# Kernel tuning notes

Hardware: AMD Instinct MI355X
Metric: run time of the kernel (lower is better)

The kernel has to match this reference:

```python
import jax, jax.numpy as jnp
import numpy as np

Q_DIM = 1024
K_DIM = 1024
HID = 128
EPS = 1e-5


def setup_inputs() -> dict:
    key = jax.random.key(0)
    ks = jax.random.split(key, 12)
    B, Tq, Tk = 2, 512, 512
    s_q = 1.0 / np.sqrt(Q_DIM)
    s_k = 1.0 / np.sqrt(K_DIM)
    s_h3 = 1.0 / np.sqrt(3 * HID)
    s_h = 1.0 / np.sqrt(HID)
    return {
        "Q": jax.random.normal(ks[0], (B, Tq, Q_DIM), jnp.float32),
        "K": jax.random.normal(ks[1], (B, Tk, K_DIM), jnp.float32),
        "Wq": jax.random.uniform(ks[2], (Q_DIM, HID), jnp.float32, -s_q, s_q),
        "Wk": jax.random.uniform(ks[3], (K_DIM, HID), jnp.float32, -s_k, s_k),
        "ln_g": jnp.ones((3 * HID,), jnp.float32),
        "ln_b": jnp.zeros((3 * HID,), jnp.float32),
        "Wu": jax.random.uniform(ks[4], (3 * HID, HID), jnp.float32, -s_h3, s_h3),
        "bu": jax.random.uniform(ks[5], (HID,), jnp.float32, -s_h3, s_h3),
        "Wv": jax.random.uniform(ks[6], (3 * HID, HID), jnp.float32, -s_h3, s_h3),
        "bv": jax.random.uniform(ks[7], (HID,), jnp.float32, -s_h3, s_h3),
        "Wo": jax.random.uniform(ks[8], (HID, 1), jnp.float32, -s_h, s_h),
        "bo": jax.random.uniform(ks[9], (1,), jnp.float32, -s_h, s_h),
    }


def reference(Q, K, Wq, Wk, ln_g, ln_b, Wu, bu, Wv, bv, Wo, bo):
    B, Tq, _ = Q.shape
    Tk = K.shape[1]
    q = jnp.einsum("bqd,dh->bqh", Q, Wq)              # (B,Tq,H)
    k = jnp.einsum("bkd,dh->bkh", K, Wk)              # (B,Tk,H)
    q_exp = jnp.broadcast_to(q[:, :, None, :], (B, Tq, Tk, HID))
    k_exp = jnp.broadcast_to(k[:, None, :, :], (B, Tq, Tk, HID))
    x = jnp.concatenate([q_exp, k_exp, q_exp * k_exp], axis=-1)  # (B,Tq,Tk,3H)
    mu = jnp.mean(x, axis=-1, keepdims=True)
    var = jnp.mean(jnp.square(x - mu), axis=-1, keepdims=True)
    x = (x - mu) * jax.lax.rsqrt(var + EPS) * ln_g + ln_b
    u = jnp.einsum("bqkc,ch->bqkh", x, Wu) + bu
    v = jnp.einsum("bqkc,ch->bqkh", x, Wv) + bv
    z = u * jax.nn.gelu(v, approximate=False)
    return (jnp.einsum("bqkh,ho->bqko", z, Wo) + bo)[..., 0]  # (B,Tq,Tk)
```

## Files before the change

kernel.cpp:

```cpp
#include <hip/hip_runtime.h>
#include <hip/hip_bf16.h>
#include <math.h>


#define EPSLN 1e-5f

#define WS_QP   0
#define WS_KP   131072
#define WS_PU   262144
#define WS_PV   393216
#define WS_RU   524288
#define WS_RV   655360
#define WS_SQ   786432
#define WS_QQ   787456
#define WS_SK   788480
#define WS_KK   789504
#define WS_GUS  790528
#define WS_GVS  790656
#define WS_CU   790784
#define WS_CV   790912
#define WS_WTU  791040
#define WS_WTV  815616
#define WS_WQT  840192
#define WS_WKT  905728

typedef __attribute__((ext_vector_type(8))) short short8;
typedef __attribute__((ext_vector_type(4))) float f32x4;

__device__ inline unsigned short f2bf(float x) {
    unsigned u = __builtin_bit_cast(unsigned, x);
    unsigned r = u + 0x7fffu + ((u >> 16) & 1u);
    return (unsigned short)(r >> 16);
}
__device__ inline float b2f_lo(unsigned v) { return __builtin_bit_cast(float, v << 16); }
__device__ inline float b2f_hi(unsigned v) { return __builtin_bit_cast(float, v & 0xffff0000u); }
__device__ inline unsigned pack_bf2(float a, float b) {
    __hip_bfloat162 h = __float22bfloat162_rn(make_float2(a, b));
    unsigned r;
    __builtin_memcpy(&r, &h, 4);
    return r;
}
__device__ inline void store8(unsigned short* p, const unsigned short* v) {
    short8 s;
    #pragma unroll
    for (int e = 0; e < 8; ++e) s[e] = (short)v[e];
    *(short8*)p = s;
}
#define GELU_C1 2.3022035f
#define GELU_C2 0.1029431f
__device__ inline float fast_gelu(float v) {
    float ex = __builtin_amdgcn_exp2f(v * fmaf(v * v, GELU_C2, GELU_C1));
    float r  = __builtin_amdgcn_rcpf(ex + 1.f);
    return v - v * r;
}
#define BAR_LDS() asm volatile("s_waitcnt lgkmcnt(0)\n\ts_barrier" ::: "memory")

__global__ __launch_bounds__(256, 2)
void k_prep(const float* __restrict__ Wu, const float* __restrict__ bu,
            const float* __restrict__ Wv, const float* __restrict__ bv,
            const float* __restrict__ g, const float* __restrict__ bln,
            const float* __restrict__ Wo,
            const float* __restrict__ Wq, const float* __restrict__ Wk,
            float* __restrict__ ws) {
    int task = blockIdx.x, t = threadIdx.x;
    if (task < 2) {
        bool isV = task != 0;
        const float* W  = isV ? Wv : Wu;
        const float* bb = isV ? bv : bu;
        float* gout = ws + (isV ? WS_GVS : WS_GUS);
        float* cout = ws + (isV ? WS_CV : WS_CU);
        __shared__ float rg[2][128], rc[2][128];
        int tl = t & 127, g2 = t >> 7;
        float gu = 0.f, cu = 0.f;
        #pragma unroll 4
        for (int c = g2 * 192; c < g2 * 192 + 192; ++c) {
            float wv_ = W[c * 128 + tl];
            gu += g[c] * wv_;
            cu += bln[c] * wv_;
        }
        rg[g2][tl] = gu; rc[g2][tl] = cu;
        __syncthreads();
        if (t < 128) gout[t] = rg[0][t] + rg[1][t];
        else { int h = t - 128; cout[h] = rc[0][h] + rc[1][h] + bb[h]; }
    } else if (task < 8) {
        int tt = task - 2;
        bool isV = tt >= 3;
        int seg = tt % 3;
        const float* W = isV ? Wv : Wu;
        unsigned short* wt = (unsigned short*)(ws + (isV ? WS_WTV : WS_WTU));
        __shared__ unsigned short tile[128 * 130];
        for (int it = 0; it < 64; ++it) {
            int idx = t + 256 * it;
            int c = idx >> 7, h = idx & 127;
            float s = g[seg * 128 + c] * (isV ? 1.f : Wo[h]);
            tile[c * 130 + h] = f2bf(s * W[(seg * 128 + c) * 128 + h]);
        }
        __syncthreads();
        int h = t >> 1, c0 = (t & 1) * 64;
        for (int cc = 0; cc < 64; cc += 8) {
            unsigned short v[8];
            #pragma unroll
            for (int e = 0; e < 8; ++e) v[e] = tile[(c0 + cc + e) * 130 + h];
            store8(&wt[h * 384 + seg * 128 + c0 + cc], v);
        }
    } else {
        int tt = task - 8;
        const float* W = (tt >> 3) ? Wk : Wq;
        unsigned short* wt = (unsigned short*)(ws + ((tt >> 3) ? WS_WKT : WS_WQT));
        int seg = tt & 7;
        __shared__ unsigned short tile[128 * 130];
        for (int it = 0; it < 64; ++it) {
            int idx = t + 256 * it;
            int c = idx >> 7, h = idx & 127;
            tile[c * 130 + h] = f2bf(W[(size_t)(seg * 128 + c) * 128 + h]);
        }
        __syncthreads();
        int h = t >> 1, c0 = (t & 1) * 64;
        for (int cc = 0; cc < 64; cc += 8) {
            unsigned short v[8];
            #pragma unroll
            for (int e = 0; e < 8; ++e) v[e] = tile[(c0 + cc + e) * 130 + h];
            store8(&wt[h * 1024 + seg * 128 + c0 + cc], v);
        }
    }
}

#define XST 1028
#define QST 132
__global__ __launch_bounds__(256, 2)
void k_proj(const float* __restrict__ Q, const float* __restrict__ K,
            float* __restrict__ ws) {
    int blk = blockIdx.x, t = threadIdx.x;
    bool isK = blk >= 128;
    int r0 = (blk & 127) * 8;
    const float* src = isK ? K : Q;
    const unsigned short* wtin = (const unsigned short*)(ws + (isK ? WS_WKT : WS_WQT));
    float* dst = ws + (isK ? WS_KP : WS_QP);
    int L = t & 63, w = t >> 6;
    int col = L & 15, quad = L >> 4;

    __shared__ unsigned short XLb[16 * XST];
    __shared__ unsigned short qpL[16 * QST];
    __shared__ float sp1[16][4], sp2[16][4];

    {
        int srow = t >> 5;
        int c0 = (t & 31) * 4;
        const float* sp = src + (size_t)(r0 + srow) * 1024;
        #pragma unroll
        for (int g8 = 0; g8 < 8; ++g8) {
            float4 xv = *(const float4*)(sp + g8 * 128 + c0);
            unsigned* xp = (unsigned*)&XLb[srow * XST + g8 * 128 + c0];
            xp[0] = pack_bf2(xv.x, xv.y);
            xp[1] = pack_bf2(xv.z, xv.w);
        }
    }
    __syncthreads();

    f32x4 acc[2];
    acc[0] = (f32x4){0.f, 0.f, 0.f, 0.f};
    acc[1] = (f32x4){0.f, 0.f, 0.f, 0.f};
    #pragma unroll 4
    for (int ks = 0; ks < 32; ++ks) {
        short8 a = *(const short8*)&XLb[col * XST + ks * 32 + quad * 8];
        #pragma unroll
        for (int nt2 = 0; nt2 < 2; ++nt2) {
            int h = w * 32 + nt2 * 16 + col;
            short8 b = *(const short8*)&wtin[(size_t)h * 1024 + ks * 32 + quad * 8];
            acc[nt2] = __builtin_amdgcn_mfma_f32_16x16x32_bf16(a, b, acc[nt2], 0, 0, 0);
        }
    }

    #pragma unroll
    for (int r = 0; r < 4; ++r) {
        int row = quad * 4 + r;
        float s1 = acc[0][r] + acc[1][r];
        float s2 = acc[0][r] * acc[0][r] + acc[1][r] * acc[1][r];
        #pragma unroll
        for (int d = 1; d < 16; d <<= 1) { s1 += __shfl_xor(s1, d); s2 += __shfl_xor(s2, d); }
        if (col == 0) { sp1[row][w] = s1; sp2[row][w] = s2; }
        #pragma unroll
        for (int nt2 = 0; nt2 < 2; ++nt2) {
            int h = w * 32 + nt2 * 16 + col;
            qpL[row * QST + h] = f2bf(acc[nt2][r]);
            if (row < 8) dst[(size_t)(r0 + row) * 128 + h] = acc[nt2][r];
        }
    }
    __syncthreads();
    if (t < 8) {
        ws[(isK ? WS_SK : WS_SQ) + r0 + t] = (sp1[t][0] + sp1[t][1]) + (sp1[t][2] + sp1[t][3]);
        ws[(isK ? WS_KK : WS_QQ) + r0 + t] = (sp2[t][0] + sp2[t][1]) + (sp2[t][2] + sp2[t][3]);
    }

    int uv = w & 1, nhf = w >> 1;
    const unsigned short* wt = (const unsigned short*)(ws + (uv ? WS_WTV : WS_WTU));
    int cb0 = isK ? 128 : 0;
    f32x4 pacc[4];
    #pragma unroll
    for (int nt = 0; nt < 4; ++nt) pacc[nt] = (f32x4){0.f, 0.f, 0.f, 0.f};
    #pragma unroll
    for (int ks = 0; ks < 4; ++ks) {
        short8 a = *(const short8*)&qpL[col * QST + ks * 32 + quad * 8];
        #pragma unroll
        for (int nt = 0; nt < 4; ++nt) {
            int h = nhf * 64 + nt * 16 + col;
            short8 b = *(const short8*)&wt[h * 384 + cb0 + ks * 32 + quad * 8];
            pacc[nt] = __builtin_amdgcn_mfma_f32_16x16x32_bf16(a, b, pacc[nt], 0, 0, 0);
        }
    }
    float* PO = ws + (uv ? (isK ? WS_RV : WS_PV) : (isK ? WS_RU : WS_PU));
    #pragma unroll
    for (int nt = 0; nt < 4; ++nt)
        #pragma unroll
        for (int r = 0; r < 4; ++r) {
            int row = quad * 4 + r;
            if (row < 8)
                PO[(size_t)(r0 + row) * 128 + nhf * 64 + nt * 16 + col] = pacc[nt][r];
        }
}

#define ASTR 152
#define REDS 132
#define PST  136
__global__ __launch_bounds__(512, 4)
void k_main(const float* __restrict__ ws, float* __restrict__ out,
            const float* __restrict__ Wo, const float* __restrict__ bo) {
    int blk = blockIdx.x;
    int jt = blk & 15, ig = (blk >> 4) & 31, b = blk >> 9;
    int t = threadIdx.x;
    int L = t & 63, w = t >> 6;
    int col = L & 15, quad = L >> 4;
    int krow0 = b * 512 + jt * 32;
    int jj = t >> 4, cb = (t & 15) * 8;
    int h = w * 16 + col;

    __shared__ __align__(16) char smem[30720];
    unsigned short* Alds = (unsigned short*)smem;
    float*          red2 = (float*)(smem + 9728);
    unsigned short* QL   = (unsigned short*)smem;
    unsigned short* Q2L  = (unsigned short*)(smem + 4352);
    unsigned short* KL   = (unsigned short*)(smem + 8704);
    unsigned short* K2L  = (unsigned short*)(smem + 17408);
    float*          rsL2 = (float*)(smem + 26624);

    int bi0 = b * 512 + ig * 16;

    float kreg[8];
    {
        const float* kp = ws + WS_KP + (size_t)(krow0 + jj) * 128 + cb;
        #pragma unroll
        for (int e = 0; e < 8; ++e) kreg[e] = kp[e];
        unsigned kk4[4], k2[4];
        #pragma unroll
        for (int e = 0; e < 4; ++e) {
            kk4[e] = pack_bf2(kreg[e * 2], kreg[e * 2 + 1]);
            k2[e]  = pack_bf2(kreg[e * 2] * kreg[e * 2], kreg[e * 2 + 1] * kreg[e * 2 + 1]);
        }
        *(uint4*)&KL[jj * PST + cb]  = *(uint4*)&kk4[0];
        *(uint4*)&K2L[jj * PST + cb] = *(uint4*)&k2[0];
    }
    {
        int row = t >> 5, c0 = (t & 31) * 4;
        float4 qv = *(const float4*)(ws + WS_QP + (size_t)(bi0 + row) * 128 + c0);
        unsigned q01 = pack_bf2(qv.x, qv.y), q23 = pack_bf2(qv.z, qv.w);
        unsigned s01 = pack_bf2(qv.x * qv.x, qv.y * qv.y);
        unsigned s23 = pack_bf2(qv.z * qv.z, qv.w * qv.w);
        uint2 qp = make_uint2(q01, q23), sp = make_uint2(s01, s23);
        *(uint2*)&QL[row * PST + c0]  = qp;
        *(uint2*)&Q2L[row * PST + c0] = sp;
    }
    unsigned prR[8];
    #pragma unroll
    for (int mt = 0; mt < 2; ++mt)
        #pragma unroll
        for (int r = 0; r < 4; ++r) {
            int jl = mt * 16 + quad * 4 + r;
            float ru = ws[WS_RU + (size_t)(krow0 + jl) * 128 + h];
            float rv = ws[WS_RV + (size_t)(krow0 + jl) * 128 + h];
            prR[mt * 4 + r] = pack_bf2(ru, rv);
        }

    short8 w3f[2][4];
    {
        const unsigned short* wtu = (const unsigned short*)(ws + WS_WTU);
        const unsigned short* wtv = (const unsigned short*)(ws + WS_WTV);
        #pragma unroll
        for (int ks = 0; ks < 4; ++ks) {
            w3f[0][ks] = *(const short8*)&wtu[h * 384 + 256 + ks * 32 + quad * 8];
            w3f[1][ks] = *(const short8*)&wtv[h * 384 + 256 + ks * 32 + quad * 8];
        }
    }
    float wo  = Wo[h];
    float gusv = ws[WS_GUS + h] * wo;
    float cuv  = ws[WS_CU + h] * wo;
    float gvsv = ws[WS_GVS + h];
    float cvv  = ws[WS_CV + h];
    float bo0 = bo[0];

    int bi = bi0;
    float4 qA = *(const float4*)(ws + WS_QP + (size_t)bi * 128 + cb);
    float4 qB = *(const float4*)(ws + WS_QP + (size_t)bi * 128 + cb + 4);
    float puv = ws[WS_PU + (size_t)bi * 128 + h];
    float pvv = ws[WS_PV + (size_t)bi * 128 + h];
    __syncthreads();

    if (w < 2) {
        int j = w * 16 + col;
        f32x4 d1a = (f32x4){0.f, 0.f, 0.f, 0.f};
        f32x4 d2a = (f32x4){0.f, 0.f, 0.f, 0.f};
        #pragma unroll
        for (int ks = 0; ks < 4; ++ks) {
            short8 aq  = *(const short8*)&QL[col * PST + ks * 32 + quad * 8];
            short8 bk  = *(const short8*)&KL[j * PST + ks * 32 + quad * 8];
            d1a = __builtin_amdgcn_mfma_f32_16x16x32_bf16(aq, bk, d1a, 0, 0, 0);
            short8 aq2 = *(const short8*)&Q2L[col * PST + ks * 32 + quad * 8];
            short8 bk2 = *(const short8*)&K2L[j * PST + ks * 32 + quad * 8];
            d2a = __builtin_amdgcn_mfma_f32_16x16x32_bf16(aq2, bk2, d2a, 0, 0, 0);
        }
        float skj = ws[WS_SK + krow0 + j];
        float kkj = ws[WS_KK + krow0 + j];
        #pragma unroll
        for (int r = 0; r < 4; ++r) {
            int i = quad * 4 + r;
            float mu = (ws[WS_SQ + bi0 + i] + skj + d1a[r]) * (1.0f / 384.0f);
            float e2 = (ws[WS_QQ + bi0 + i] + kkj + d2a[r]) * (1.0f / 384.0f);
            float rs = rsqrtf(e2 - mu * mu + EPSLN);
            *(float2*)&rsL2[(i * 32 + j) * 2] = make_float2(rs, rs * mu);
        }
    }
    __syncthreads();

    #pragma unroll 2
    for (int ii = 0; ii < 16; ++ii) {
        int bin = bi0 + ((ii + 1) & 15);
        float4 qA2 = *(const float4*)(ws + WS_QP + (size_t)bin * 128 + cb);
        float4 qB2 = *(const float4*)(ws + WS_QP + (size_t)bin * 128 + cb + 4);
        float pu2 = ws[WS_PU + (size_t)bin * 128 + h];
        float pv2 = ws[WS_PV + (size_t)bin * 128 + h];
        {
            unsigned pk[4];
            float x0 = kreg[0] * qA.x, x1 = kreg[1] * qA.y;
            float x2 = kreg[2] * qA.z, x3 = kreg[3] * qA.w;
            float y0 = kreg[4] * qB.x, y1 = kreg[5] * qB.y;
            float y2 = kreg[6] * qB.z, y3 = kreg[7] * qB.w;
            pk[0] = pack_bf2(x0, x1); pk[1] = pack_bf2(x2, x3);
            pk[2] = pack_bf2(y0, y1); pk[3] = pack_bf2(y2, y3);
            unsigned* arow = (unsigned*)Alds + jj * (ASTR / 2) + cb / 2;
            *(uint4*)&arow[0] = *(uint4*)&pk[0];
        }
        BAR_LDS();
        f32x4 acc[2][2];
        #pragma unroll
        for (int mt = 0; mt < 2; ++mt) {
            acc[mt][0] = (f32x4){puv, puv, puv, puv};
            acc[mt][1] = (f32x4){pvv, pvv, pvv, pvv};
        }
        #pragma unroll
        for (int ks = 0; ks < 4; ++ks) {
            short8 a0 = *(const short8*)&Alds[col * ASTR + ks * 32 + quad * 8];
            short8 a1 = *(const short8*)&Alds[(col + 16) * ASTR + ks * 32 + quad * 8];
            acc[0][0] = __builtin_amdgcn_mfma_f32_16x16x32_bf16(a0, w3f[0][ks], acc[0][0], 0, 0, 0);
            acc[0][1] = __builtin_amdgcn_mfma_f32_16x16x32_bf16(a0, w3f[1][ks], acc[0][1], 0, 0, 0);
            acc[1][0] = __builtin_amdgcn_mfma_f32_16x16x32_bf16(a1, w3f[0][ks], acc[1][0], 0, 0, 0);
            acc[1][1] = __builtin_amdgcn_mfma_f32_16x16x32_bf16(a1, w3f[1][ks], acc[1][1], 0, 0, 0);
        }
        #pragma unroll
        for (int mt = 0; mt < 2; ++mt) {
            float4 s0 = *(const float4*)&rsL2[(ii * 32 + mt * 16 + quad * 4) * 2];
            float4 s1 = *(const float4*)&rsL2[(ii * 32 + mt * 16 + quad * 4) * 2 + 4];
            #pragma unroll
            for (int r = 0; r < 4; ++r) {
                float rs   = r == 0 ? s0.x : r == 1 ? s0.z : r == 2 ? s1.x : s1.z;
                float rsmu = r == 0 ? s0.y : r == 1 ? s0.w : r == 2 ? s1.y : s1.w;
                int jl = mt * 16 + quad * 4 + r;
                unsigned pr = prR[mt * 4 + r];
                float su  = acc[mt][0][r] + b2f_lo(pr);
                float u   = fmaf(rs, su, fmaf(-rsmu, gusv, cuv));
                float sv_ = acc[mt][1][r] + b2f_hi(pr);
                float v   = fmaf(rs, sv_, fmaf(-rsmu, gvsv, cvv));
                red2[jl * REDS + w * 16 + col] = u * fast_gelu(v);
            }
        }
        BAR_LDS();
        if (t < 256) {
            const float4* rr = (const float4*)&red2[(t >> 3) * REDS];
            int k = t & 7;
            float s = 0.f;
            #pragma unroll
            for (int c4 = 0; c4 < 4; ++c4) {
                float4 x = rr[k + c4 * 8];
                s += (x.x + x.y) + (x.z + x.w);
            }
            s += __shfl_xor(s, 1);
            s += __shfl_xor(s, 2);
            s += __shfl_xor(s, 4);
            if (k == 0)
                out[(size_t)bi * 512 + jt * 32 + (t >> 3)] = s + bo0;
        }
        qA = qA2; qB = qB2; puv = pu2; pvv = pv2; bi = bin;
    }
}

extern "C" void kernel_launch(void* const* d_in, const int* in_sizes, int n_in,
                              void* d_out, int out_size, void* d_ws, size_t ws_size,
                              hipStream_t stream) {
    const float* Q   = (const float*)d_in[0];
    const float* K   = (const float*)d_in[1];
    const float* Wq  = (const float*)d_in[2];
    const float* Wk  = (const float*)d_in[3];
    const float* g   = (const float*)d_in[4];
    const float* bln = (const float*)d_in[5];
    const float* Wu  = (const float*)d_in[6];
    const float* bu  = (const float*)d_in[7];
    const float* Wv  = (const float*)d_in[8];
    const float* bv  = (const float*)d_in[9];
    const float* Wo  = (const float*)d_in[10];
    const float* bo  = (const float*)d_in[11];
    float* ws  = (float*)d_ws;
    float* out = (float*)d_out;

    hipLaunchKernelGGL(k_prep, dim3(24), dim3(256), 0, stream, Wu, bu, Wv, bv, g, bln, Wo, Wq, Wk, ws);
    hipLaunchKernelGGL(k_proj, dim3(256), dim3(256), 0, stream, Q, K, ws);
    hipLaunchKernelGGL(k_main, dim3(1024), dim3(512), 0, stream, ws, out, Wo, bo);
}
```

Before: 183.4 us.

## Double key tile per block to 64 with 1024-thread blocks

Each k_main block now covers 64 key rows instead of 32. It uses 16 waves, split into two key halves of 8 hidden-dim waves each, and twice the LDS. The grid is halved, so per-row Q/PU/PV loads, the LayerNorm statistics MFMA and the setup work are amortized over twice as many keys. In exchange, each block barrier now spans 16 waves, LDS per block grows to 60KB, and the prefetch on the last iteration now reads one row past the tile instead of wrapping back to the first row.

```diff
diff --git a/kernel.cpp b/kernel.cpp
--- a/kernel.cpp
+++ b/kernel.cpp
@@ -222,26 +222,27 @@
 #define ASTR 152
 #define REDS 132
 #define PST  136
-__global__ __launch_bounds__(512, 4)
+__global__ __launch_bounds__(1024, 4)
 void k_main(const float* __restrict__ ws, float* __restrict__ out,
             const float* __restrict__ Wo, const float* __restrict__ bo) {
     int blk = blockIdx.x;
-    int jt = blk & 15, ig = (blk >> 4) & 31, b = blk >> 9;
+    int jt = blk & 7, ig = (blk >> 3) & 31, b = blk >> 8;
     int t = threadIdx.x;
     int L = t & 63, w = t >> 6;
     int col = L & 15, quad = L >> 4;
-    int krow0 = b * 512 + jt * 32;
+    int jh = w >> 3, wh = w & 7;
+    int krow0 = b * 512 + jt * 64;
     int jj = t >> 4, cb = (t & 15) * 8;
-    int h = w * 16 + col;
-
-    __shared__ __align__(16) char smem[30720];
+    int h = wh * 16 + col;
+
+    __shared__ __align__(16) char smem[61440];
     unsigned short* Alds = (unsigned short*)smem;
-    float*          red2 = (float*)(smem + 9728);
+    float*          red2 = (float*)(smem + 19456);
     unsigned short* QL   = (unsigned short*)smem;
     unsigned short* Q2L  = (unsigned short*)(smem + 4352);
     unsigned short* KL   = (unsigned short*)(smem + 8704);
-    unsigned short* K2L  = (unsigned short*)(smem + 17408);
-    float*          rsL2 = (float*)(smem + 26624);
+    unsigned short* K2L  = (unsigned short*)(smem + 26112);
+    float*          rsL2 = (float*)(smem + 53248);
 
     int bi0 = b * 512 + ig * 16;
 
@@ -259,7 +260,7 @@
         *(uint4*)&KL[jj * PST + cb]  = *(uint4*)&kk4[0];
         *(uint4*)&K2L[jj * PST + cb] = *(uint4*)&k2[0];
     }
-    {
+    if (t < 512) {
         int row = t >> 5, c0 = (t & 31) * 4;
         float4 qv = *(const float4*)(ws + WS_QP + (size_t)(bi0 + row) * 128 + c0);
         unsigned q01 = pack_bf2(qv.x, qv.y), q23 = pack_bf2(qv.z, qv.w);
@@ -274,7 +275,7 @@
     for (int mt = 0; mt < 2; ++mt)
         #pragma unroll
         for (int r = 0; r < 4; ++r) {
-            int jl = mt * 16 + quad * 4 + r;
+            int jl = jh * 32 + mt * 16 + quad * 4 + r;
             float ru = ws[WS_RU + (size_t)(krow0 + jl) * 128 + h];
             float rv = ws[WS_RV + (size_t)(krow0 + jl) * 128 + h];
             prR[mt * 4 + r] = pack_bf2(ru, rv);
@@ -297,14 +298,16 @@
     float cvv  = ws[WS_CV + h];
     float bo0 = bo[0];
 
-    int bi = bi0;
-    float4 qA = *(const float4*)(ws + WS_QP + (size_t)bi * 128 + cb);
-    float4 qB = *(const float4*)(ws + WS_QP + (size_t)bi * 128 + cb + 4);
-    float puv = ws[WS_PU + (size_t)bi * 128 + h];
-    float pvv = ws[WS_PV + (size_t)bi * 128 + h];
+    const float* qpBase = ws + WS_QP + (size_t)bi0 * 128 + cb;
+    const float* puBase = ws + WS_PU + (size_t)bi0 * 128 + h;
+    const float* pvBase = ws + WS_PV + (size_t)bi0 * 128 + h;
+    float4 qA = *(const float4*)(qpBase);
+    float4 qB = *(const float4*)(qpBase + 4);
+    float puv = puBase[0];
+    float pvv = pvBase[0];
     __syncthreads();
 
-    if (w < 2) {
+    if (w < 4) {
         int j = w * 16 + col;
         f32x4 d1a = (f32x4){0.f, 0.f, 0.f, 0.f};
         f32x4 d2a = (f32x4){0.f, 0.f, 0.f, 0.f};
@@ -325,18 +328,17 @@
             float mu = (ws[WS_SQ + bi0 + i] + skj + d1a[r]) * (1.0f / 384.0f);
             float e2 = (ws[WS_QQ + bi0 + i] + kkj + d2a[r]) * (1.0f / 384.0f);
             float rs = rsqrtf(e2 - mu * mu + EPSLN);
-            *(float2*)&rsL2[(i * 32 + j) * 2] = make_float2(rs, rs * mu);
+            *(float2*)&rsL2[(i * 64 + j) * 2] = make_float2(rs, rs * mu);
         }
     }
     __syncthreads();
 
     #pragma unroll 2
     for (int ii = 0; ii < 16; ++ii) {
-        int bin = bi0 + ((ii + 1) & 15);
-        float4 qA2 = *(const float4*)(ws + WS_QP + (size_t)bin * 128 + cb);
-        float4 qB2 = *(const float4*)(ws + WS_QP + (size_t)bin * 128 + cb + 4);
-        float pu2 = ws[WS_PU + (size_t)bin * 128 + h];
-        float pv2 = ws[WS_PV + (size_t)bin * 128 + h];
+        float4 qA2 = *(const float4*)(qpBase + (ii + 1) * 128);
+        float4 qB2 = *(const float4*)(qpBase + (ii + 1) * 128 + 4);
+        float pu2 = puBase[(ii + 1) * 128];
+        float pv2 = pvBase[(ii + 1) * 128];
         {
             unsigned pk[4];
             float x0 = kreg[0] * qA.x, x1 = kreg[1] * qA.y;
@@ -357,8 +359,8 @@
         }
         #pragma unroll
         for (int ks = 0; ks < 4; ++ks) {
-            short8 a0 = *(const short8*)&Alds[col * ASTR + ks * 32 + quad * 8];
-            short8 a1 = *(const short8*)&Alds[(col + 16) * ASTR + ks * 32 + quad * 8];
+            short8 a0 = *(const short8*)&Alds[(jh * 32 + col) * ASTR + ks * 32 + quad * 8];
+            short8 a1 = *(const short8*)&Alds[(jh * 32 + col + 16) * ASTR + ks * 32 + quad * 8];
             acc[0][0] = __builtin_amdgcn_mfma_f32_16x16x32_bf16(a0, w3f[0][ks], acc[0][0], 0, 0, 0);
             acc[0][1] = __builtin_amdgcn_mfma_f32_16x16x32_bf16(a0, w3f[1][ks], acc[0][1], 0, 0, 0);
             acc[1][0] = __builtin_amdgcn_mfma_f32_16x16x32_bf16(a1, w3f[0][ks], acc[1][0], 0, 0, 0);
@@ -366,23 +368,24 @@
         }
         #pragma unroll
         for (int mt = 0; mt < 2; ++mt) {
-            float4 s0 = *(const float4*)&rsL2[(ii * 32 + mt * 16 + quad * 4) * 2];
-            float4 s1 = *(const float4*)&rsL2[(ii * 32 + mt * 16 + quad * 4) * 2 + 4];
+            int jb = jh * 32 + mt * 16 + quad * 4;
+            float4 s0 = *(const float4*)&rsL2[(ii * 64 + jb) * 2];
+            float4 s1 = *(const float4*)&rsL2[(ii * 64 + jb) * 2 + 4];
             #pragma unroll
             for (int r = 0; r < 4; ++r) {
                 float rs   = r == 0 ? s0.x : r == 1 ? s0.z : r == 2 ? s1.x : s1.z;
                 float rsmu = r == 0 ? s0.y : r == 1 ? s0.w : r == 2 ? s1.y : s1.w;
-                int jl = mt * 16 + quad * 4 + r;
+                int jl = jb + r;
                 unsigned pr = prR[mt * 4 + r];
                 float su  = acc[mt][0][r] + b2f_lo(pr);
                 float u   = fmaf(rs, su, fmaf(-rsmu, gusv, cuv));
                 float sv_ = acc[mt][1][r] + b2f_hi(pr);
                 float v   = fmaf(rs, sv_, fmaf(-rsmu, gvsv, cvv));
-                red2[jl * REDS + w * 16 + col] = u * fast_gelu(v);
+                red2[jl * REDS + wh * 16 + col] = u * fast_gelu(v);
             }
         }
         BAR_LDS();
-        if (t < 256) {
+        if (t < 512) {
             const float4* rr = (const float4*)&red2[(t >> 3) * REDS];
             int k = t & 7;
             float s = 0.f;
@@ -395,9 +398,9 @@
             s += __shfl_xor(s, 2);
             s += __shfl_xor(s, 4);
             if (k == 0)
-                out[(size_t)bi * 512 + jt * 32 + (t >> 3)] = s + bo0;
-        }
-        qA = qA2; qB = qB2; puv = pu2; pvv = pv2; bi = bin;
+                out[(size_t)(bi0 + ii) * 512 + jt * 64 + (t >> 3)] = s + bo0;
+        }
+        qA = qA2; qB = qB2; puv = pu2; pvv = pv2;
     }
 }
 
@@ -421,5 +424,5 @@
 
     hipLaunchKernelGGL(k_prep, dim3(24), dim3(256), 0, stream, Wu, bu, Wv, bv, g, bln, Wo, Wq, Wk, ws);
     hipLaunchKernelGGL(k_proj, dim3(256), dim3(256), 0, stream, Q, K, ws);
-    hipLaunchKernelGGL(k_main, dim3(1024), dim3(512), 0, stream, ws, out, Wo, bo);
-}
+    hipLaunchKernelGGL(k_main, dim3(512), dim3(1024), 0, stream, ws, out, Wo, bo);
+}
```

After: 187.4 us. 1.02x slower.
